# Kernel tuning notes

Measured on AMD Instinct MI355X. Metric: run time of the kernel, lower is better.

## Reference

```python
import jax, jax.numpy as jnp
import numpy as np

N = 100000
E = 1600000
BN_EPS = 1e-5
L2_EPS = 1e-12


def _sage_conv(x, src, dst, wl, bl, wr):
    # mean-aggregate source features onto destination nodes
    s = jax.ops.segment_sum(x[src], dst, num_segments=N)          # [N, C]
    cnt = jax.ops.segment_sum(jnp.ones((E,), x.dtype), dst, num_segments=N)
    agg = s / jnp.maximum(cnt, 1.0)[:, None]
    out = agg @ wl.T + bl + x @ wr.T                              # lin_l(agg) + lin_r(x)
    # normalize=True -> row-wise L2 normalization
    nrm = jnp.sqrt(jnp.sum(out * out, axis=-1, keepdims=True))
    return out / jnp.maximum(nrm, L2_EPS)


def _bn(x, g, b):
    # BatchNorm1d, training-mode batch statistics (biased variance)
    m = jnp.mean(x, axis=0)
    v = jnp.mean((x - m) ** 2, axis=0)
    return (x - m) / jnp.sqrt(v + BN_EPS) * g + b


def setup_inputs() -> dict:
    key = jax.random.key(0)
    ks = jax.random.split(key, 24)
    dims = [(4, 6), (6, 8), (8, 16), (16, 32)]
    inp = {
        "x": jax.random.normal(ks[0], (N, 4), jnp.float32),
        "edge_index": jax.random.randint(ks[1], (2, E), 0, N, dtype=jnp.int64),
    }
    ki = 2
    for li, (ci, co) in enumerate(dims, start=1):
        sc = 1.0 / np.sqrt(ci)
        inp[f"w{li}l"] = jax.random.uniform(ks[ki], (co, ci), jnp.float32, -sc, sc); ki += 1
        inp[f"b{li}l"] = jax.random.uniform(ks[ki], (co,), jnp.float32, -sc, sc); ki += 1
        inp[f"w{li}r"] = jax.random.uniform(ks[ki], (co, ci), jnp.float32, -sc, sc); ki += 1
    for li, co in enumerate([6, 8, 16], start=1):
        inp[f"g{li}"] = jnp.ones((co,), jnp.float32)
        inp[f"be{li}"] = jnp.zeros((co,), jnp.float32)
    return inp


def reference(x, edge_index,
              w1l, b1l, w1r, w2l, b2l, w2r, w3l, b3l, w3r, w4l, b4l, w4r,
              g1, be1, g2, be2, g3, be3):
    src, dst = edge_index[0], edge_index[1]
    h = _sage_conv(x, src, dst, w1l, b1l, w1r)
    h = _bn(jax.nn.relu(h), g1, be1)
    h = _sage_conv(h, src, dst, w2l, b2l, w2r)
    h = _bn(jax.nn.relu(h), g2, be2)
    h = _sage_conv(h, src, dst, w3l, b3l, w3r)
    h = _bn(jax.nn.relu(h), g3, be3)
    h = _sage_conv(h, src, dst, w4l, b4l, w4r)
    return jax.nn.relu(h)
```

## Files before the change

kernel.cpp:

```cpp
#include <hip/hip_runtime.h>

#define NNODES 100000
#define NEDGES 1600000
#define BN_EPS 1e-5f
#define L2_EPS 1e-12f

#define BKT_SHIFT 9
#define BKT_SIZE  512
#define NBKT      196
#define CHUNK     4096
#define NBLK_E    391

__global__ void hist_kernel(const int* __restrict__ dst,
                            int* __restrict__ blk_hist, float* __restrict__ stats) {
    __shared__ int h[NBKT];
    for (int i = threadIdx.x; i < NBKT; i += blockDim.x) h[i] = 0;
    if (blockIdx.x == 0 && threadIdx.x < 128) {
        stats[threadIdx.x] = 0.0f;
        stats[threadIdx.x + 128] = 0.0f;
        stats[threadIdx.x + 256] = 0.0f;
    }
    __syncthreads();
    int base = blockIdx.x * CHUNK;
    int end  = min(base + CHUNK, NEDGES);
    for (int e = base + threadIdx.x; e < end; e += blockDim.x)
        atomicAdd(&h[dst[e] >> BKT_SHIFT], 1);
    __syncthreads();
    for (int i = threadIdx.x; i < NBKT; i += blockDim.x)
        blk_hist[blockIdx.x * NBKT + i] = h[i];
}

__global__ void scan_blocks(const int* __restrict__ blk_hist,
                            int* __restrict__ blk_off, int* __restrict__ bucket_total) {
    __shared__ int tmp[512];
    int b = blockIdx.x;
    int i = threadIdx.x;
    int v = (i < NBLK_E) ? blk_hist[i * NBKT + b] : 0;
    tmp[i] = v;
    __syncthreads();
    for (int off = 1; off < 512; off <<= 1) {
        int t = (i >= off) ? tmp[i - off] : 0;
        __syncthreads();
        tmp[i] += t;
        __syncthreads();
    }
    if (i < NBLK_E) blk_off[i * NBKT + b] = tmp[i] - v;
    if (i == 511) bucket_total[b] = tmp[511];
}

__global__ void scan_buckets(const int* __restrict__ bucket_total, int* __restrict__ bucket_base) {
    __shared__ int tmp[256];
    int v = (threadIdx.x < NBKT) ? bucket_total[threadIdx.x] : 0;
    tmp[threadIdx.x] = v;
    __syncthreads();
    for (int off = 1; off < 256; off <<= 1) {
        int t = (threadIdx.x >= off) ? tmp[threadIdx.x - off] : 0;
        __syncthreads();
        tmp[threadIdx.x] += t;
        __syncthreads();
    }
    if (threadIdx.x < NBKT) bucket_base[threadIdx.x] = tmp[threadIdx.x] - v;
    if (threadIdx.x == 0) bucket_base[NBKT] = NEDGES;
}

__global__ void bucket_scatter(const int* __restrict__ src, const int* __restrict__ dst,
                               const int* __restrict__ blk_off, const int* __restrict__ bucket_base,
                               unsigned int* __restrict__ staged) {
    __shared__ int cur[NBKT];
    for (int i = threadIdx.x; i < NBKT; i += blockDim.x)
        cur[i] = blk_off[blockIdx.x * NBKT + i] + bucket_base[i];
    __syncthreads();
    int base = blockIdx.x * CHUNK;
    int end  = min(base + CHUNK, NEDGES);
    for (int e = base + threadIdx.x; e < end; e += blockDim.x) {
        int d = dst[e];
        int b = d >> BKT_SHIFT;
        int p = atomicAdd(&cur[b], 1);
        staged[p] = ((unsigned)(d & (BKT_SIZE - 1)) << 23) | (unsigned)src[e];
    }
}

__global__ void csr_finalize(const unsigned int* __restrict__ staged,
                             const int* __restrict__ bucket_base,
                             int* __restrict__ row_ptr, int* __restrict__ col) {
    __shared__ int nh[BKT_SIZE];
    __shared__ int cur[BKT_SIZE];
    int b = blockIdx.x;
    int beg = bucket_base[b], end = bucket_base[b + 1];

    nh[threadIdx.x] = 0;
    __syncthreads();
    for (int e = beg + threadIdx.x; e < end; e += blockDim.x)
        atomicAdd(&nh[staged[e] >> 23], 1);
    __syncthreads();

    int v = nh[threadIdx.x];
    cur[threadIdx.x] = v;
    __syncthreads();
    for (int off = 1; off < 512; off <<= 1) {
        int t = (threadIdx.x >= off) ? cur[threadIdx.x - off] : 0;
        __syncthreads();
        cur[threadIdx.x] += t;
        __syncthreads();
    }
    int excl = cur[threadIdx.x] - v;

    int node = b * BKT_SIZE + threadIdx.x;
    if (node < NNODES) row_ptr[node] = beg + excl;
    if (b == 0 && threadIdx.x == 0) row_ptr[NNODES] = NEDGES;
    __syncthreads();
    cur[threadIdx.x] = excl;
    __syncthreads();

    for (int e = beg + threadIdx.x; e < end; e += blockDim.x) {
        unsigned pk = staged[e];
        int l = (int)(pk >> 23);
        int p = atomicAdd(&cur[l], 1);
        col[beg + p] = (int)(pk & 0x7FFFFF);
    }
}

template<int CI>
__device__ __forceinline__ void load_row(const float* __restrict__ p, float* r) {
    constexpr int N4 = CI / 4;
#pragma unroll
    for (int i = 0; i < N4; i++) {
        float4 v = ((const float4*)p)[i];
        r[4*i] = v.x; r[4*i+1] = v.y; r[4*i+2] = v.z; r[4*i+3] = v.w;
    }
    if constexpr ((CI % 4) >= 2) {
        float2 v = ((const float2*)(p + 4 * N4))[0];
        r[4*N4] = v.x; r[4*N4+1] = v.y;
    }
    if constexpr ((CI % 2) == 1) r[CI - 1] = p[CI - 1];
}

template<int CI, int SI, int CO, int SO, int G, bool IN_AFFINE, bool DO_STATS>
__global__ void layer_kernel(const int* __restrict__ row_ptr, const int* __restrict__ col,
                             const float* __restrict__ h,
                             const float* __restrict__ ssum_in, const float* __restrict__ ssq_in,
                             const float* __restrict__ g_in, const float* __restrict__ b_in,
                             const float* __restrict__ wl, const float* __restrict__ bl,
                             const float* __restrict__ wr,
                             float* __restrict__ y,
                             float* __restrict__ stat_sum, float* __restrict__ stat_sq) {
    constexpr int NPB = 256 / G;
    constexpr int OPL = (CO + G - 1) / G;
    constexpr int PCI = CI + 1;

    __shared__ float sWl[CO * PCI];
    __shared__ float sWr[CO * PCI];
    __shared__ float sBl[CO];
    __shared__ float sSc[CI];
    __shared__ float sSh[CI];
    __shared__ float red_sum[CO];
    __shared__ float red_sq[CO];

    for (int i = threadIdx.x; i < CO * CI; i += blockDim.x) {
        int o = i / CI, c = i - o * CI;
        sWl[o * PCI + c] = wl[i];
        sWr[o * PCI + c] = wr[i];
    }
    if (threadIdx.x < CO) {
        sBl[threadIdx.x] = bl[threadIdx.x];
        if (DO_STATS) { red_sum[threadIdx.x] = 0.0f; red_sq[threadIdx.x] = 0.0f; }
    }
    if (IN_AFFINE && threadIdx.x < CI) {
        float m  = ssum_in[threadIdx.x] * (1.0f / NNODES);
        float vv = ssq_in[threadIdx.x] * (1.0f / NNODES) - m * m;
        float s  = g_in[threadIdx.x] / sqrtf(vv + BN_EPS);
        sSc[threadIdx.x] = s;
        sSh[threadIdx.x] = b_in[threadIdx.x] - m * s;
    }
    __syncthreads();

    int node = blockIdx.x * NPB + (threadIdx.x / G);
    int g    = threadIdx.x & (G - 1);
    bool valid = node < NNODES;

    float acc[CI];
#pragma unroll
    for (int c = 0; c < CI; c++) acc[c] = 0.0f;

    int beg = 0, end = 0;
    if (valid) {
        beg = row_ptr[node];
        end = row_ptr[node + 1];
        int j = beg + g;
        for (; j + 3 * G < end; j += 4 * G) {
            int i0 = col[j], i1 = col[j + G], i2 = col[j + 2 * G], i3 = col[j + 3 * G];
            float r0[CI], r1[CI], r2[CI], r3[CI];
            load_row<CI>(h + (long)i0 * SI, r0);
            load_row<CI>(h + (long)i1 * SI, r1);
            load_row<CI>(h + (long)i2 * SI, r2);
            load_row<CI>(h + (long)i3 * SI, r3);
#pragma unroll
            for (int c = 0; c < CI; c++) acc[c] += (r0[c] + r1[c]) + (r2[c] + r3[c]);
        }
        for (; j + G < end; j += 2 * G) {
            int i0 = col[j], i1 = col[j + G];
            float r0[CI], r1[CI];
            load_row<CI>(h + (long)i0 * SI, r0);
            load_row<CI>(h + (long)i1 * SI, r1);
#pragma unroll
            for (int c = 0; c < CI; c++) acc[c] += r0[c] + r1[c];
        }
        if (j < end) {
            float r0[CI];
            load_row<CI>(h + (long)col[j] * SI, r0);
#pragma unroll
            for (int c = 0; c < CI; c++) acc[c] += r0[c];
        }
    }

#pragma unroll
    for (int m = 1; m < G; m <<= 1)
#pragma unroll
        for (int c = 0; c < CI; c++) acc[c] += __shfl_xor(acc[c], m);

    float out[OPL];
    float nrm2 = 0.0f;
    if (valid) {
        float ic = 1.0f / fmaxf((float)(end - beg), 1.0f);
        float xin[CI];
        load_row<CI>(h + (long)node * SI, xin);
        float agg[CI];
#pragma unroll
        for (int c = 0; c < CI; c++) {
            float a  = acc[c] * ic;
            float xv = xin[c];
            if (IN_AFFINE) {
                a  = a  * sSc[c] + sSh[c];
                xv = xv * sSc[c] + sSh[c];
            }
            agg[c] = a;
            xin[c] = xv;
        }
#pragma unroll
        for (int k = 0; k < OPL; k++) {
            int o = g * OPL + k;
            float v = 0.0f;
            if (o < CO) {
                v = sBl[o];
#pragma unroll
                for (int c = 0; c < CI; c++)
                    v += sWl[o * PCI + c] * agg[c] + sWr[o * PCI + c] * xin[c];
            }
            out[k] = v;
            nrm2 += v * v;
        }
    }
#pragma unroll
    for (int m = 1; m < G; m <<= 1) nrm2 += __shfl_xor(nrm2, m);

    if (valid) {
        float inv_nrm = 1.0f / fmaxf(sqrtf(nrm2), L2_EPS);
#pragma unroll
        for (int k = 0; k < OPL; k++) {
            int o = g * OPL + k;
            if (o < CO) {
                float v = fmaxf(out[k] * inv_nrm, 0.0f);
                y[(long)node * SO + o] = v;
                if (DO_STATS) {
                    atomicAdd(&red_sum[o], v);
                    atomicAdd(&red_sq[o], v * v);
                }
            }
        }
    }

    if (DO_STATS) {
        __syncthreads();
        if (threadIdx.x < CO) {
            atomicAdd(&stat_sum[threadIdx.x], red_sum[threadIdx.x]);
            atomicAdd(&stat_sq[threadIdx.x], red_sq[threadIdx.x]);
        }
    }
}

extern "C" void kernel_launch(void* const* d_in, const int* in_sizes, int n_in,
                              void* d_out, int out_size, void* d_ws, size_t ws_size,
                              hipStream_t stream) {
    const float* x   = (const float*)d_in[0];
    const int*   ei  = (const int*)d_in[1];
    const int*   src = ei;
    const int*   dst = ei + NEDGES;

    const float* w1l = (const float*)d_in[2];
    const float* b1l = (const float*)d_in[3];
    const float* w1r = (const float*)d_in[4];
    const float* w2l = (const float*)d_in[5];
    const float* b2l = (const float*)d_in[6];
    const float* w2r = (const float*)d_in[7];
    const float* w3l = (const float*)d_in[8];
    const float* b3l = (const float*)d_in[9];
    const float* w3r = (const float*)d_in[10];
    const float* w4l = (const float*)d_in[11];
    const float* b4l = (const float*)d_in[12];
    const float* w4r = (const float*)d_in[13];
    const float* g1  = (const float*)d_in[14];
    const float* be1 = (const float*)d_in[15];
    const float* g2  = (const float*)d_in[16];
    const float* be2 = (const float*)d_in[17];
    const float* g3  = (const float*)d_in[18];
    const float* be3 = (const float*)d_in[19];

    char* w = (char*)d_ws;
    int* blk_hist     = (int*)w;  w += NBLK_E * NBKT * 4;
    int* blk_off      = (int*)w;  w += NBLK_E * NBKT * 4;
    int* bucket_total = (int*)w;  w += 256 * 4;
    int* bucket_base  = (int*)w;  w += 256 * 4;
    int* row_ptr      = (int*)w;  w += (NNODES + 8) * 4;
    int* col          = (int*)w;  w += NEDGES * 4;
    float* hA         = (float*)w; w += NNODES * 16 * 4;
    float* hB         = (float*)w; w += NNODES * 16 * 4;
    float* stats      = (float*)w; w += 3 * 128 * 4;
    unsigned int* staged = (unsigned int*)hB;

    float* ssum1 = stats + 0 * 128, *ssq1 = ssum1 + 32;
    float* ssum2 = stats + 1 * 128, *ssq2 = ssum2 + 32;
    float* ssum3 = stats + 2 * 128, *ssq3 = ssum3 + 32;

    hist_kernel   <<<NBLK_E, 256, 0, stream>>>(dst, blk_hist, stats);
    scan_blocks   <<<NBKT, 512, 0, stream>>>(blk_hist, blk_off, bucket_total);
    scan_buckets  <<<1, 256, 0, stream>>>(bucket_total, bucket_base);
    bucket_scatter<<<NBLK_E, 256, 0, stream>>>(src, dst, blk_off, bucket_base, staged);
    csr_finalize  <<<NBKT, 512, 0, stream>>>(staged, bucket_base, row_ptr, col);

    layer_kernel<4, 4, 6, 8, 4, false, true><<<(NNODES * 4 + 255) / 256, 256, 0, stream>>>(
        row_ptr, col, x, nullptr, nullptr, nullptr, nullptr,
        w1l, b1l, w1r, hA, ssum1, ssq1);

    layer_kernel<6, 8, 8, 8, 4, true, true><<<(NNODES * 4 + 255) / 256, 256, 0, stream>>>(
        row_ptr, col, hA, ssum1, ssq1, g1, be1,
        w2l, b2l, w2r, hB, ssum2, ssq2);

    layer_kernel<8, 8, 16, 16, 4, true, true><<<(NNODES * 4 + 255) / 256, 256, 0, stream>>>(
        row_ptr, col, hB, ssum2, ssq2, g2, be2,
        w3l, b3l, w3r, hA, ssum3, ssq3);

    layer_kernel<16, 16, 32, 32, 8, true, false><<<(NNODES * 8 + 255) / 256, 256, 0, stream>>>(
        row_ptr, col, hA, ssum3, ssq3, g3, be3,
        w4l, b4l, w4r, (float*)d_out, nullptr, nullptr);
}
```

Baseline: 276.4 us.

## Reorder nodes by in-degree within buckets to balance gather work

The CSR finalize kernel now counting-sorts the nodes of each 512-node bucket by in-degree and writes a permutation array. Each layer kernel maps its thread groups through this permutation, so groups in the same wavefront handle nodes with similar degrees and loop divergence drops. The cost is an extra indirection load per node, scattered output writes and row_ptr reads, and some extra shared-memory scan work in csr_finalize.

```diff
diff --git a/kernel.cpp b/kernel.cpp
--- a/kernel.cpp
+++ b/kernel.cpp
@@ -82,13 +82,17 @@
 
 __global__ void csr_finalize(const unsigned int* __restrict__ staged,
                              const int* __restrict__ bucket_base,
-                             int* __restrict__ row_ptr, int* __restrict__ col) {
+                             int* __restrict__ row_ptr, int* __restrict__ col,
+                             int* __restrict__ perm) {
     __shared__ int nh[BKT_SIZE];
     __shared__ int cur[BKT_SIZE];
+    __shared__ int dh[128];
+    __shared__ int dcur[128];
     int b = blockIdx.x;
     int beg = bucket_base[b], end = bucket_base[b + 1];
 
     nh[threadIdx.x] = 0;
+    if (threadIdx.x < 128) dh[threadIdx.x] = 0;
     __syncthreads();
     for (int e = beg + threadIdx.x; e < end; e += blockDim.x)
         atomicAdd(&nh[staged[e] >> 23], 1);
@@ -106,7 +110,8 @@
     int excl = cur[threadIdx.x] - v;
 
     int node = b * BKT_SIZE + threadIdx.x;
-    if (node < NNODES) row_ptr[node] = beg + excl;
+    bool node_valid = node < NNODES;
+    if (node_valid) row_ptr[node] = beg + excl;
     if (b == 0 && threadIdx.x == 0) row_ptr[NNODES] = NEDGES;
     __syncthreads();
     cur[threadIdx.x] = excl;
@@ -118,6 +123,24 @@
         int p = atomicAdd(&cur[l], 1);
         col[beg + p] = (int)(pk & 0x7FFFFF);
     }
+
+    int bin = min(v, 127);
+    if (node_valid) atomicAdd(&dh[bin], 1);
+    __syncthreads();
+    if (threadIdx.x < 128) dcur[threadIdx.x] = dh[threadIdx.x];
+    __syncthreads();
+    for (int off = 1; off < 128; off <<= 1) {
+        int t = (threadIdx.x < 128 && threadIdx.x >= off) ? dcur[threadIdx.x - off] : 0;
+        __syncthreads();
+        if (threadIdx.x < 128) dcur[threadIdx.x] += t;
+        __syncthreads();
+    }
+    if (threadIdx.x < 128) dcur[threadIdx.x] -= dh[threadIdx.x];
+    __syncthreads();
+    if (node_valid) {
+        int pos = atomicAdd(&dcur[bin], 1);
+        perm[b * BKT_SIZE + pos] = node;
+    }
 }
 
 template<int CI>
@@ -137,6 +160,7 @@
 
 template<int CI, int SI, int CO, int SO, int G, bool IN_AFFINE, bool DO_STATS>
 __global__ void layer_kernel(const int* __restrict__ row_ptr, const int* __restrict__ col,
+                             const int* __restrict__ perm,
                              const float* __restrict__ h,
                              const float* __restrict__ ssum_in, const float* __restrict__ ssq_in,
                              const float* __restrict__ g_in, const float* __restrict__ b_in,
@@ -174,9 +198,10 @@
     }
     __syncthreads();
 
-    int node = blockIdx.x * NPB + (threadIdx.x / G);
+    int gid  = blockIdx.x * NPB + (threadIdx.x / G);
     int g    = threadIdx.x & (G - 1);
-    bool valid = node < NNODES;
+    bool valid = gid < NNODES;
+    int node = valid ? perm[gid] : 0;
 
     float acc[CI];
 #pragma unroll
@@ -311,6 +336,7 @@
     int* bucket_total = (int*)w;  w += 256 * 4;
     int* bucket_base  = (int*)w;  w += 256 * 4;
     int* row_ptr      = (int*)w;  w += (NNODES + 8) * 4;
+    int* perm         = (int*)w;  w += NBKT * BKT_SIZE * 4;
     int* col          = (int*)w;  w += NEDGES * 4;
     float* hA         = (float*)w; w += NNODES * 16 * 4;
     float* hB         = (float*)w; w += NNODES * 16 * 4;
@@ -325,21 +351,21 @@
     scan_blocks   <<<NBKT, 512, 0, stream>>>(blk_hist, blk_off, bucket_total);
     scan_buckets  <<<1, 256, 0, stream>>>(bucket_total, bucket_base);
     bucket_scatter<<<NBLK_E, 256, 0, stream>>>(src, dst, blk_off, bucket_base, staged);
-    csr_finalize  <<<NBKT, 512, 0, stream>>>(staged, bucket_base, row_ptr, col);
+    csr_finalize  <<<NBKT, 512, 0, stream>>>(staged, bucket_base, row_ptr, col, perm);
 
     layer_kernel<4, 4, 6, 8, 4, false, true><<<(NNODES * 4 + 255) / 256, 256, 0, stream>>>(
-        row_ptr, col, x, nullptr, nullptr, nullptr, nullptr,
+        row_ptr, col, perm, x, nullptr, nullptr, nullptr, nullptr,
         w1l, b1l, w1r, hA, ssum1, ssq1);
 
     layer_kernel<6, 8, 8, 8, 4, true, true><<<(NNODES * 4 + 255) / 256, 256, 0, stream>>>(
-        row_ptr, col, hA, ssum1, ssq1, g1, be1,
+        row_ptr, col, perm, hA, ssum1, ssq1, g1, be1,
         w2l, b2l, w2r, hB, ssum2, ssq2);
 
     layer_kernel<8, 8, 16, 16, 4, true, true><<<(NNODES * 4 + 255) / 256, 256, 0, stream>>>(
-        row_ptr, col, hB, ssum2, ssq2, g2, be2,
+        row_ptr, col, perm, hB, ssum2, ssq2, g2, be2,
         w3l, b3l, w3r, hA, ssum3, ssq3);
 
     layer_kernel<16, 16, 32, 32, 8, true, false><<<(NNODES * 8 + 255) / 256, 256, 0, stream>>>(
-        row_ptr, col, hA, ssum3, ssq3, g3, be3,
+        row_ptr, col, perm, hA, ssum3, ssq3, g3, be3,
         w4l, b4l, w4r, (float*)d_out, nullptr, nullptr);
 }
```

After: 292.8 us. +5.9%, slower.

## Replace CSR build with bucketed edge lists and shared-memory atomic aggregation

Applied to the files above, without the earlier changes.

The per-node CSR finalize pass is dropped. Edges are bucketed into groups of 128 destination nodes, and each layer kernel walks the bucket's packed (local dst, src) list, accumulating neighbor features into a shared-memory tile with LDS float atomics. A small kernel precomputes inverse degrees. This removes the col/row_ptr construction and the sort within each bucket, but it adds heavy LDS atomic contention, only 782 blocks per layer, and an epilogue where only half the threads do the dense transform with one thread per node.

```diff
diff --git a/kernel.cpp b/kernel.cpp
--- a/kernel.cpp
+++ b/kernel.cpp
@@ -5,9 +5,9 @@
 #define BN_EPS 1e-5f
 #define L2_EPS 1e-12f
 
-#define BKT_SHIFT 9
-#define BKT_SIZE  512
-#define NBKT      196
+#define BKT_SHIFT 7
+#define BKT_SIZE  128
+#define NBKT      782
 #define CHUNK     4096
 #define NBLK_E    391
 
@@ -49,11 +49,11 @@
 }
 
 __global__ void scan_buckets(const int* __restrict__ bucket_total, int* __restrict__ bucket_base) {
-    __shared__ int tmp[256];
+    __shared__ int tmp[1024];
     int v = (threadIdx.x < NBKT) ? bucket_total[threadIdx.x] : 0;
     tmp[threadIdx.x] = v;
     __syncthreads();
-    for (int off = 1; off < 256; off <<= 1) {
+    for (int off = 1; off < 1024; off <<= 1) {
         int t = (threadIdx.x >= off) ? tmp[threadIdx.x - off] : 0;
         __syncthreads();
         tmp[threadIdx.x] += t;
@@ -76,67 +76,58 @@
         int d = dst[e];
         int b = d >> BKT_SHIFT;
         int p = atomicAdd(&cur[b], 1);
-        staged[p] = ((unsigned)(d & (BKT_SIZE - 1)) << 23) | (unsigned)src[e];
-    }
-}
-
-__global__ void csr_finalize(const unsigned int* __restrict__ staged,
-                             const int* __restrict__ bucket_base,
-                             int* __restrict__ row_ptr, int* __restrict__ col) {
-    __shared__ int nh[BKT_SIZE];
-    __shared__ int cur[BKT_SIZE];
+        staged[p] = ((unsigned)(d & (BKT_SIZE - 1)) << 25) | (unsigned)src[e];
+    }
+}
+
+__global__ void invdeg_kernel(const unsigned int* __restrict__ staged,
+                              const int* __restrict__ bucket_base,
+                              float* __restrict__ invdeg) {
+    __shared__ int deg[BKT_SIZE];
     int b = blockIdx.x;
+    if (threadIdx.x < BKT_SIZE) deg[threadIdx.x] = 0;
+    __syncthreads();
     int beg = bucket_base[b], end = bucket_base[b + 1];
-
-    nh[threadIdx.x] = 0;
-    __syncthreads();
     for (int e = beg + threadIdx.x; e < end; e += blockDim.x)
-        atomicAdd(&nh[staged[e] >> 23], 1);
-    __syncthreads();
-
-    int v = nh[threadIdx.x];
-    cur[threadIdx.x] = v;
-    __syncthreads();
-    for (int off = 1; off < 512; off <<= 1) {
-        int t = (threadIdx.x >= off) ? cur[threadIdx.x - off] : 0;
-        __syncthreads();
-        cur[threadIdx.x] += t;
-        __syncthreads();
-    }
-    int excl = cur[threadIdx.x] - v;
-
-    int node = b * BKT_SIZE + threadIdx.x;
-    if (node < NNODES) row_ptr[node] = beg + excl;
-    if (b == 0 && threadIdx.x == 0) row_ptr[NNODES] = NEDGES;
-    __syncthreads();
-    cur[threadIdx.x] = excl;
-    __syncthreads();
-
-    for (int e = beg + threadIdx.x; e < end; e += blockDim.x) {
-        unsigned pk = staged[e];
-        int l = (int)(pk >> 23);
-        int p = atomicAdd(&cur[l], 1);
-        col[beg + p] = (int)(pk & 0x7FFFFF);
-    }
-}
-
-template<int CI>
+        atomicAdd(&deg[staged[e] >> 25], 1);
+    __syncthreads();
+    if (threadIdx.x < BKT_SIZE) {
+        int node = b * BKT_SIZE + threadIdx.x;
+        if (node < NNODES)
+            invdeg[node] = 1.0f / fmaxf((float)deg[threadIdx.x], 1.0f);
+    }
+}
+
+template<int C>
 __device__ __forceinline__ void load_row(const float* __restrict__ p, float* r) {
-    constexpr int N4 = CI / 4;
+    constexpr int N4 = C / 4;
 #pragma unroll
     for (int i = 0; i < N4; i++) {
         float4 v = ((const float4*)p)[i];
         r[4*i] = v.x; r[4*i+1] = v.y; r[4*i+2] = v.z; r[4*i+3] = v.w;
     }
-    if constexpr ((CI % 4) >= 2) {
+    if constexpr ((C % 4) >= 2) {
         float2 v = ((const float2*)(p + 4 * N4))[0];
         r[4*N4] = v.x; r[4*N4+1] = v.y;
     }
-    if constexpr ((CI % 2) == 1) r[CI - 1] = p[CI - 1];
-}
-
-template<int CI, int SI, int CO, int SO, int G, bool IN_AFFINE, bool DO_STATS>
-__global__ void layer_kernel(const int* __restrict__ row_ptr, const int* __restrict__ col,
+    if constexpr ((C % 2) == 1) r[C - 1] = p[C - 1];
+}
+
+template<int C>
+__device__ __forceinline__ void store_row(float* __restrict__ p, const float* r) {
+    constexpr int N4 = C / 4;
+#pragma unroll
+    for (int i = 0; i < N4; i++)
+        ((float4*)p)[i] = make_float4(r[4*i], r[4*i+1], r[4*i+2], r[4*i+3]);
+    if constexpr ((C % 4) >= 2)
+        ((float2*)(p + 4 * N4))[0] = make_float2(r[4*N4], r[4*N4+1]);
+    if constexpr ((C % 2) == 1) p[C - 1] = r[C - 1];
+}
+
+template<int CI, int SI, int CO, int SO, bool IN_AFFINE, bool DO_STATS>
+__global__ void layer_kernel(const unsigned int* __restrict__ staged,
+                             const int* __restrict__ bucket_base,
+                             const float* __restrict__ invdeg,
                              const float* __restrict__ h,
                              const float* __restrict__ ssum_in, const float* __restrict__ ssq_in,
                              const float* __restrict__ g_in, const float* __restrict__ b_in,
@@ -144,10 +135,9 @@
                              const float* __restrict__ wr,
                              float* __restrict__ y,
                              float* __restrict__ stat_sum, float* __restrict__ stat_sq) {
-    constexpr int NPB = 256 / G;
-    constexpr int OPL = (CO + G - 1) / G;
     constexpr int PCI = CI + 1;
 
+    __shared__ float agg[BKT_SIZE * PCI];
     __shared__ float sWl[CO * PCI];
     __shared__ float sWr[CO * PCI];
     __shared__ float sBl[CO];
@@ -156,6 +146,7 @@
     __shared__ float red_sum[CO];
     __shared__ float red_sq[CO];
 
+    for (int i = threadIdx.x; i < BKT_SIZE * PCI; i += blockDim.x) agg[i] = 0.0f;
     for (int i = threadIdx.x; i < CO * CI; i += blockDim.x) {
         int o = i / CI, c = i - o * CI;
         sWl[o * PCI + c] = wl[i];
@@ -174,98 +165,77 @@
     }
     __syncthreads();
 
-    int node = blockIdx.x * NPB + (threadIdx.x / G);
-    int g    = threadIdx.x & (G - 1);
-    bool valid = node < NNODES;
-
-    float acc[CI];
-#pragma unroll
-    for (int c = 0; c < CI; c++) acc[c] = 0.0f;
-
-    int beg = 0, end = 0;
-    if (valid) {
-        beg = row_ptr[node];
-        end = row_ptr[node + 1];
-        int j = beg + g;
-        for (; j + 3 * G < end; j += 4 * G) {
-            int i0 = col[j], i1 = col[j + G], i2 = col[j + 2 * G], i3 = col[j + 3 * G];
-            float r0[CI], r1[CI], r2[CI], r3[CI];
-            load_row<CI>(h + (long)i0 * SI, r0);
-            load_row<CI>(h + (long)i1 * SI, r1);
-            load_row<CI>(h + (long)i2 * SI, r2);
-            load_row<CI>(h + (long)i3 * SI, r3);
-#pragma unroll
-            for (int c = 0; c < CI; c++) acc[c] += (r0[c] + r1[c]) + (r2[c] + r3[c]);
-        }
-        for (; j + G < end; j += 2 * G) {
-            int i0 = col[j], i1 = col[j + G];
-            float r0[CI], r1[CI];
-            load_row<CI>(h + (long)i0 * SI, r0);
-            load_row<CI>(h + (long)i1 * SI, r1);
-#pragma unroll
-            for (int c = 0; c < CI; c++) acc[c] += r0[c] + r1[c];
-        }
-        if (j < end) {
-            float r0[CI];
-            load_row<CI>(h + (long)col[j] * SI, r0);
-#pragma unroll
-            for (int c = 0; c < CI; c++) acc[c] += r0[c];
-        }
-    }
-
-#pragma unroll
-    for (int m = 1; m < G; m <<= 1)
-#pragma unroll
-        for (int c = 0; c < CI; c++) acc[c] += __shfl_xor(acc[c], m);
-
-    float out[OPL];
-    float nrm2 = 0.0f;
-    if (valid) {
-        float ic = 1.0f / fmaxf((float)(end - beg), 1.0f);
-        float xin[CI];
-        load_row<CI>(h + (long)node * SI, xin);
-        float agg[CI];
-#pragma unroll
-        for (int c = 0; c < CI; c++) {
-            float a  = acc[c] * ic;
-            float xv = xin[c];
-            if (IN_AFFINE) {
-                a  = a  * sSc[c] + sSh[c];
-                xv = xv * sSc[c] + sSh[c];
+    int b   = blockIdx.x;
+    int beg = bucket_base[b], end = bucket_base[b + 1];
+
+    int j = beg + threadIdx.x;
+    for (; j + 3 * 256 < end; j += 4 * 256) {
+        unsigned pk0 = staged[j], pk1 = staged[j + 256],
+                 pk2 = staged[j + 512], pk3 = staged[j + 768];
+        float r0[CI], r1[CI], r2[CI], r3[CI];
+        load_row<CI>(h + (long)(pk0 & 0x1FFFFFFu) * SI, r0);
+        load_row<CI>(h + (long)(pk1 & 0x1FFFFFFu) * SI, r1);
+        load_row<CI>(h + (long)(pk2 & 0x1FFFFFFu) * SI, r2);
+        load_row<CI>(h + (long)(pk3 & 0x1FFFFFFu) * SI, r3);
+        int l0 = pk0 >> 25, l1 = pk1 >> 25, l2 = pk2 >> 25, l3 = pk3 >> 25;
+#pragma unroll
+        for (int c = 0; c < CI; c++) atomicAdd(&agg[l0 * PCI + c], r0[c]);
+#pragma unroll
+        for (int c = 0; c < CI; c++) atomicAdd(&agg[l1 * PCI + c], r1[c]);
+#pragma unroll
+        for (int c = 0; c < CI; c++) atomicAdd(&agg[l2 * PCI + c], r2[c]);
+#pragma unroll
+        for (int c = 0; c < CI; c++) atomicAdd(&agg[l3 * PCI + c], r3[c]);
+    }
+    for (; j < end; j += 256) {
+        unsigned pk = staged[j];
+        float r0[CI];
+        load_row<CI>(h + (long)(pk & 0x1FFFFFFu) * SI, r0);
+        int l = pk >> 25;
+#pragma unroll
+        for (int c = 0; c < CI; c++) atomicAdd(&agg[l * PCI + c], r0[c]);
+    }
+    __syncthreads();
+
+    if (threadIdx.x < BKT_SIZE) {
+        int node = b * BKT_SIZE + threadIdx.x;
+        if (node < NNODES) {
+            float ic = invdeg[node];
+            float xin[CI], ag[CI];
+            load_row<CI>(h + (long)node * SI, xin);
+#pragma unroll
+            for (int c = 0; c < CI; c++) {
+                float a  = agg[threadIdx.x * PCI + c] * ic;
+                float xv = xin[c];
+                if (IN_AFFINE) {
+                    a  = a  * sSc[c] + sSh[c];
+                    xv = xv * sSc[c] + sSh[c];
+                }
+                ag[c]  = a;
+                xin[c] = xv;
             }
-            agg[c] = a;
-            xin[c] = xv;
-        }
-#pragma unroll
-        for (int k = 0; k < OPL; k++) {
-            int o = g * OPL + k;
-            float v = 0.0f;
-            if (o < CO) {
-                v = sBl[o];
+            float out[CO];
+            float nrm2 = 0.0f;
+#pragma unroll
+            for (int o = 0; o < CO; o++) {
+                float v = sBl[o];
 #pragma unroll
                 for (int c = 0; c < CI; c++)
-                    v += sWl[o * PCI + c] * agg[c] + sWr[o * PCI + c] * xin[c];
+                    v += sWl[o * PCI + c] * ag[c] + sWr[o * PCI + c] * xin[c];
+                out[o] = v;
+                nrm2 += v * v;
             }
-            out[k] = v;
-            nrm2 += v * v;
-        }
-    }
-#pragma unroll
-    for (int m = 1; m < G; m <<= 1) nrm2 += __shfl_xor(nrm2, m);
-
-    if (valid) {
-        float inv_nrm = 1.0f / fmaxf(sqrtf(nrm2), L2_EPS);
-#pragma unroll
-        for (int k = 0; k < OPL; k++) {
-            int o = g * OPL + k;
-            if (o < CO) {
-                float v = fmaxf(out[k] * inv_nrm, 0.0f);
-                y[(long)node * SO + o] = v;
+            float inv_nrm = 1.0f / fmaxf(sqrtf(nrm2), L2_EPS);
+#pragma unroll
+            for (int o = 0; o < CO; o++) {
+                float v = fmaxf(out[o] * inv_nrm, 0.0f);
+                out[o] = v;
                 if (DO_STATS) {
                     atomicAdd(&red_sum[o], v);
                     atomicAdd(&red_sq[o], v * v);
                 }
             }
+            store_row<CO>(y + (long)node * SO, out);
         }
     }
 
@@ -308,14 +278,13 @@
     char* w = (char*)d_ws;
     int* blk_hist     = (int*)w;  w += NBLK_E * NBKT * 4;
     int* blk_off      = (int*)w;  w += NBLK_E * NBKT * 4;
-    int* bucket_total = (int*)w;  w += 256 * 4;
-    int* bucket_base  = (int*)w;  w += 256 * 4;
-    int* row_ptr      = (int*)w;  w += (NNODES + 8) * 4;
-    int* col          = (int*)w;  w += NEDGES * 4;
+    int* bucket_total = (int*)w;  w += 1024 * 4;
+    int* bucket_base  = (int*)w;  w += 1024 * 4;
+    float* invdeg     = (float*)w; w += NNODES * 4;
+    unsigned int* staged = (unsigned int*)w; w += NEDGES * 4;
     float* hA         = (float*)w; w += NNODES * 16 * 4;
     float* hB         = (float*)w; w += NNODES * 16 * 4;
     float* stats      = (float*)w; w += 3 * 128 * 4;
-    unsigned int* staged = (unsigned int*)hB;
 
     float* ssum1 = stats + 0 * 128, *ssq1 = ssum1 + 32;
     float* ssum2 = stats + 1 * 128, *ssq2 = ssum2 + 32;
@@ -323,23 +292,23 @@
 
     hist_kernel   <<<NBLK_E, 256, 0, stream>>>(dst, blk_hist, stats);
     scan_blocks   <<<NBKT, 512, 0, stream>>>(blk_hist, blk_off, bucket_total);
-    scan_buckets  <<<1, 256, 0, stream>>>(bucket_total, bucket_base);
+    scan_buckets  <<<1, 1024, 0, stream>>>(bucket_total, bucket_base);
     bucket_scatter<<<NBLK_E, 256, 0, stream>>>(src, dst, blk_off, bucket_base, staged);
-    csr_finalize  <<<NBKT, 512, 0, stream>>>(staged, bucket_base, row_ptr, col);
-
-    layer_kernel<4, 4, 6, 8, 4, false, true><<<(NNODES * 4 + 255) / 256, 256, 0, stream>>>(
-        row_ptr, col, x, nullptr, nullptr, nullptr, nullptr,
+    invdeg_kernel <<<NBKT, 256, 0, stream>>>(staged, bucket_base, invdeg);
+
+    layer_kernel<4, 4, 6, 8, false, true><<<NBKT, 256, 0, stream>>>(
+        staged, bucket_base, invdeg, x, nullptr, nullptr, nullptr, nullptr,
         w1l, b1l, w1r, hA, ssum1, ssq1);
 
-    layer_kernel<6, 8, 8, 8, 4, true, true><<<(NNODES * 4 + 255) / 256, 256, 0, stream>>>(
-        row_ptr, col, hA, ssum1, ssq1, g1, be1,
+    layer_kernel<6, 8, 8, 8, true, true><<<NBKT, 256, 0, stream>>>(
+        staged, bucket_base, invdeg, hA, ssum1, ssq1, g1, be1,
         w2l, b2l, w2r, hB, ssum2, ssq2);
 
-    layer_kernel<8, 8, 16, 16, 4, true, true><<<(NNODES * 4 + 255) / 256, 256, 0, stream>>>(
-        row_ptr, col, hB, ssum2, ssq2, g2, be2,
+    layer_kernel<8, 8, 16, 16, true, true><<<NBKT, 256, 0, stream>>>(
+        staged, bucket_base, invdeg, hB, ssum2, ssq2, g2, be2,
         w3l, b3l, w3r, hA, ssum3, ssq3);
 
-    layer_kernel<16, 16, 32, 32, 8, true, false><<<(NNODES * 8 + 255) / 256, 256, 0, stream>>>(
-        row_ptr, col, hA, ssum3, ssq3, g3, be3,
+    layer_kernel<16, 16, 32, 32, true, false><<<NBKT, 256, 0, stream>>>(
+        staged, bucket_base, invdeg, hA, ssum3, ssq3, g3, be3,
         w4l, b4l, w4r, (float*)d_out, nullptr, nullptr);
 }
```

New measurement: 654.5 us. +136.8%, slower.

## Fuse four SAGE layer launches into one cooperative persistent kernel

Applied to the files above, without the earlier changes.

Replaces the four per-layer kernel launches with a single cooperative kernel that runs each layer in a grid-stride loop and separates layers with grid-wide syncs. This aims to remove the launch gaps and tail drain between layers. Per-block BN stat reductions now accumulate over many node tiles before the global atomic flush. It risks lower occupancy from combined shared memory and adds grid-sync cost, and it keeps the old multi-launch path as a fallback.

```diff
diff --git a/kernel.cpp b/kernel.cpp
--- a/kernel.cpp
+++ b/kernel.cpp
@@ -1,4 +1,7 @@
 #include <hip/hip_runtime.h>
+#include <hip/hip_cooperative_groups.h>
+
+namespace cg = cooperative_groups;
 
 #define NNODES 100000
 #define NEDGES 1600000
@@ -133,6 +136,153 @@
         r[4*N4] = v.x; r[4*N4+1] = v.y;
     }
     if constexpr ((CI % 2) == 1) r[CI - 1] = p[CI - 1];
+}
+
+template<int CI, int SI, int CO, int SO, int G, bool IN_AFFINE, bool DO_STATS>
+__device__ void layer_body(const int* __restrict__ row_ptr, const int* __restrict__ col,
+                           const float* __restrict__ h,
+                           const float* __restrict__ ssum_in, const float* __restrict__ ssq_in,
+                           const float* __restrict__ g_in, const float* __restrict__ b_in,
+                           const float* __restrict__ wl, const float* __restrict__ bl,
+                           const float* __restrict__ wr,
+                           float* __restrict__ y,
+                           float* __restrict__ stat_sum, float* __restrict__ stat_sq) {
+    constexpr int NPB = 256 / G;
+    constexpr int OPL = (CO + G - 1) / G;
+    constexpr int PCI = CI + 1;
+
+    __shared__ float sWl[CO * PCI];
+    __shared__ float sWr[CO * PCI];
+    __shared__ float sBl[CO];
+    __shared__ float sSc[CI];
+    __shared__ float sSh[CI];
+    __shared__ float red_sum[CO];
+    __shared__ float red_sq[CO];
+
+    for (int i = threadIdx.x; i < CO * CI; i += 256) {
+        int o = i / CI, c = i - o * CI;
+        sWl[o * PCI + c] = wl[i];
+        sWr[o * PCI + c] = wr[i];
+    }
+    if (threadIdx.x < CO) {
+        sBl[threadIdx.x] = bl[threadIdx.x];
+        if (DO_STATS) { red_sum[threadIdx.x] = 0.0f; red_sq[threadIdx.x] = 0.0f; }
+    }
+    if (IN_AFFINE && threadIdx.x < CI) {
+        float m  = ssum_in[threadIdx.x] * (1.0f / NNODES);
+        float vv = ssq_in[threadIdx.x] * (1.0f / NNODES) - m * m;
+        float s  = g_in[threadIdx.x] / sqrtf(vv + BN_EPS);
+        sSc[threadIdx.x] = s;
+        sSh[threadIdx.x] = b_in[threadIdx.x] - m * s;
+    }
+    __syncthreads();
+
+    const int NITER = (NNODES + NPB - 1) / NPB;
+    int g = threadIdx.x & (G - 1);
+
+    for (int vb = blockIdx.x; vb < NITER; vb += gridDim.x) {
+        int node = vb * NPB + (threadIdx.x / G);
+        bool valid = node < NNODES;
+
+        float acc[CI];
+#pragma unroll
+        for (int c = 0; c < CI; c++) acc[c] = 0.0f;
+
+        int beg = 0, end = 0;
+        if (valid) {
+            beg = row_ptr[node];
+            end = row_ptr[node + 1];
+            int j = beg + g;
+            for (; j + 3 * G < end; j += 4 * G) {
+                int i0 = col[j], i1 = col[j + G], i2 = col[j + 2 * G], i3 = col[j + 3 * G];
+                float r0[CI], r1[CI], r2[CI], r3[CI];
+                load_row<CI>(h + (long)i0 * SI, r0);
+                load_row<CI>(h + (long)i1 * SI, r1);
+                load_row<CI>(h + (long)i2 * SI, r2);
+                load_row<CI>(h + (long)i3 * SI, r3);
+#pragma unroll
+                for (int c = 0; c < CI; c++) acc[c] += (r0[c] + r1[c]) + (r2[c] + r3[c]);
+            }
+            for (; j + G < end; j += 2 * G) {
+                int i0 = col[j], i1 = col[j + G];
+                float r0[CI], r1[CI];
+                load_row<CI>(h + (long)i0 * SI, r0);
+                load_row<CI>(h + (long)i1 * SI, r1);
+#pragma unroll
+                for (int c = 0; c < CI; c++) acc[c] += r0[c] + r1[c];
+            }
+            if (j < end) {
+                float r0[CI];
+                load_row<CI>(h + (long)col[j] * SI, r0);
+#pragma unroll
+                for (int c = 0; c < CI; c++) acc[c] += r0[c];
+            }
+        }
+
+#pragma unroll
+        for (int m = 1; m < G; m <<= 1)
+#pragma unroll
+            for (int c = 0; c < CI; c++) acc[c] += __shfl_xor(acc[c], m);
+
+        float out[OPL];
+        float nrm2 = 0.0f;
+        if (valid) {
+            float ic = 1.0f / fmaxf((float)(end - beg), 1.0f);
+            float xin[CI];
+            load_row<CI>(h + (long)node * SI, xin);
+            float agg[CI];
+#pragma unroll
+            for (int c = 0; c < CI; c++) {
+                float a  = acc[c] * ic;
+                float xv = xin[c];
+                if (IN_AFFINE) {
+                    a  = a  * sSc[c] + sSh[c];
+                    xv = xv * sSc[c] + sSh[c];
+                }
+                agg[c] = a;
+                xin[c] = xv;
+            }
+#pragma unroll
+            for (int k = 0; k < OPL; k++) {
+                int o = g * OPL + k;
+                float v = 0.0f;
+                if (o < CO) {
+                    v = sBl[o];
+#pragma unroll
+                    for (int c = 0; c < CI; c++)
+                        v += sWl[o * PCI + c] * agg[c] + sWr[o * PCI + c] * xin[c];
+                }
+                out[k] = v;
+                nrm2 += v * v;
+            }
+        }
+#pragma unroll
+        for (int m = 1; m < G; m <<= 1) nrm2 += __shfl_xor(nrm2, m);
+
+        if (valid) {
+            float inv_nrm = 1.0f / fmaxf(sqrtf(nrm2), L2_EPS);
+#pragma unroll
+            for (int k = 0; k < OPL; k++) {
+                int o = g * OPL + k;
+                if (o < CO) {
+                    float v = fmaxf(out[k] * inv_nrm, 0.0f);
+                    y[(long)node * SO + o] = v;
+                    if (DO_STATS) {
+                        atomicAdd(&red_sum[o], v);
+                        atomicAdd(&red_sq[o], v * v);
+                    }
+                }
+            }
+        }
+    }
+
+    if (DO_STATS) {
+        __syncthreads();
+        if (threadIdx.x < CO) {
+            atomicAdd(&stat_sum[threadIdx.x], red_sum[threadIdx.x]);
+            atomicAdd(&stat_sq[threadIdx.x], red_sq[threadIdx.x]);
+        }
+    }
 }
 
 template<int CI, int SI, int CO, int SO, int G, bool IN_AFFINE, bool DO_STATS>
@@ -144,138 +294,52 @@
                              const float* __restrict__ wr,
                              float* __restrict__ y,
                              float* __restrict__ stat_sum, float* __restrict__ stat_sq) {
-    constexpr int NPB = 256 / G;
-    constexpr int OPL = (CO + G - 1) / G;
-    constexpr int PCI = CI + 1;
-
-    __shared__ float sWl[CO * PCI];
-    __shared__ float sWr[CO * PCI];
-    __shared__ float sBl[CO];
-    __shared__ float sSc[CI];
-    __shared__ float sSh[CI];
-    __shared__ float red_sum[CO];
-    __shared__ float red_sq[CO];
-
-    for (int i = threadIdx.x; i < CO * CI; i += blockDim.x) {
-        int o = i / CI, c = i - o * CI;
-        sWl[o * PCI + c] = wl[i];
-        sWr[o * PCI + c] = wr[i];
-    }
-    if (threadIdx.x < CO) {
-        sBl[threadIdx.x] = bl[threadIdx.x];
-        if (DO_STATS) { red_sum[threadIdx.x] = 0.0f; red_sq[threadIdx.x] = 0.0f; }
-    }
-    if (IN_AFFINE && threadIdx.x < CI) {
-        float m  = ssum_in[threadIdx.x] * (1.0f / NNODES);
-        float vv = ssq_in[threadIdx.x] * (1.0f / NNODES) - m * m;
-        float s  = g_in[threadIdx.x] / sqrtf(vv + BN_EPS);
-        sSc[threadIdx.x] = s;
-        sSh[threadIdx.x] = b_in[threadIdx.x] - m * s;
-    }
-    __syncthreads();
-
-    int node = blockIdx.x * NPB + (threadIdx.x / G);
-    int g    = threadIdx.x & (G - 1);
-    bool valid = node < NNODES;
-
-    float acc[CI];
-#pragma unroll
-    for (int c = 0; c < CI; c++) acc[c] = 0.0f;
-
-    int beg = 0, end = 0;
-    if (valid) {
-        beg = row_ptr[node];
-        end = row_ptr[node + 1];
-        int j = beg + g;
-        for (; j + 3 * G < end; j += 4 * G) {
-            int i0 = col[j], i1 = col[j + G], i2 = col[j + 2 * G], i3 = col[j + 3 * G];
-            float r0[CI], r1[CI], r2[CI], r3[CI];
-            load_row<CI>(h + (long)i0 * SI, r0);
-            load_row<CI>(h + (long)i1 * SI, r1);
-            load_row<CI>(h + (long)i2 * SI, r2);
-            load_row<CI>(h + (long)i3 * SI, r3);
-#pragma unroll
-            for (int c = 0; c < CI; c++) acc[c] += (r0[c] + r1[c]) + (r2[c] + r3[c]);
-        }
-        for (; j + G < end; j += 2 * G) {
-            int i0 = col[j], i1 = col[j + G];
-            float r0[CI], r1[CI];
-            load_row<CI>(h + (long)i0 * SI, r0);
-            load_row<CI>(h + (long)i1 * SI, r1);
-#pragma unroll
-            for (int c = 0; c < CI; c++) acc[c] += r0[c] + r1[c];
-        }
-        if (j < end) {
-            float r0[CI];
-            load_row<CI>(h + (long)col[j] * SI, r0);
-#pragma unroll
-            for (int c = 0; c < CI; c++) acc[c] += r0[c];
-        }
-    }
-
-#pragma unroll
-    for (int m = 1; m < G; m <<= 1)
-#pragma unroll
-        for (int c = 0; c < CI; c++) acc[c] += __shfl_xor(acc[c], m);
-
-    float out[OPL];
-    float nrm2 = 0.0f;
-    if (valid) {
-        float ic = 1.0f / fmaxf((float)(end - beg), 1.0f);
-        float xin[CI];
-        load_row<CI>(h + (long)node * SI, xin);
-        float agg[CI];
-#pragma unroll
-        for (int c = 0; c < CI; c++) {
-            float a  = acc[c] * ic;
-            float xv = xin[c];
-            if (IN_AFFINE) {
-                a  = a  * sSc[c] + sSh[c];
-                xv = xv * sSc[c] + sSh[c];
-            }
-            agg[c] = a;
-            xin[c] = xv;
-        }
-#pragma unroll
-        for (int k = 0; k < OPL; k++) {
-            int o = g * OPL + k;
-            float v = 0.0f;
-            if (o < CO) {
-                v = sBl[o];
-#pragma unroll
-                for (int c = 0; c < CI; c++)
-                    v += sWl[o * PCI + c] * agg[c] + sWr[o * PCI + c] * xin[c];
-            }
-            out[k] = v;
-            nrm2 += v * v;
-        }
-    }
-#pragma unroll
-    for (int m = 1; m < G; m <<= 1) nrm2 += __shfl_xor(nrm2, m);
-
-    if (valid) {
-        float inv_nrm = 1.0f / fmaxf(sqrtf(nrm2), L2_EPS);
-#pragma unroll
-        for (int k = 0; k < OPL; k++) {
-            int o = g * OPL + k;
-            if (o < CO) {
-                float v = fmaxf(out[k] * inv_nrm, 0.0f);
-                y[(long)node * SO + o] = v;
-                if (DO_STATS) {
-                    atomicAdd(&red_sum[o], v);
-                    atomicAdd(&red_sq[o], v * v);
-                }
-            }
-        }
-    }
-
-    if (DO_STATS) {
-        __syncthreads();
-        if (threadIdx.x < CO) {
-            atomicAdd(&stat_sum[threadIdx.x], red_sum[threadIdx.x]);
-            atomicAdd(&stat_sq[threadIdx.x], red_sq[threadIdx.x]);
-        }
-    }
+    layer_body<CI, SI, CO, SO, G, IN_AFFINE, DO_STATS>(
+        row_ptr, col, h, ssum_in, ssq_in, g_in, b_in, wl, bl, wr, y, stat_sum, stat_sq);
+}
+
+struct KParams {
+    const int* row_ptr; const int* col;
+    const float* x;
+    float* hA; float* hB;
+    float* stats;
+    const float* w1l; const float* b1l; const float* w1r;
+    const float* w2l; const float* b2l; const float* w2r;
+    const float* w3l; const float* b3l; const float* w3r;
+    const float* w4l; const float* b4l; const float* w4r;
+    const float* g1; const float* be1;
+    const float* g2; const float* be2;
+    const float* g3; const float* be3;
+    float* out;
+};
+
+__global__ void fused_layers(KParams p) {
+    cg::grid_group grid = cg::this_grid();
+    float* ssum1 = p.stats + 0 * 128, *ssq1 = ssum1 + 32;
+    float* ssum2 = p.stats + 1 * 128, *ssq2 = ssum2 + 32;
+    float* ssum3 = p.stats + 2 * 128, *ssq3 = ssum3 + 32;
+
+    layer_body<4, 4, 6, 8, 4, false, true>(
+        p.row_ptr, p.col, p.x, nullptr, nullptr, nullptr, nullptr,
+        p.w1l, p.b1l, p.w1r, p.hA, ssum1, ssq1);
+    __threadfence();
+    grid.sync();
+
+    layer_body<6, 8, 8, 8, 4, true, true>(
+        p.row_ptr, p.col, p.hA, ssum1, ssq1, p.g1, p.be1,
+        p.w2l, p.b2l, p.w2r, p.hB, ssum2, ssq2);
+    __threadfence();
+    grid.sync();
+
+    layer_body<8, 8, 16, 16, 4, true, true>(
+        p.row_ptr, p.col, p.hB, ssum2, ssq2, p.g2, p.be2,
+        p.w3l, p.b3l, p.w3r, p.hA, ssum3, ssq3);
+    __threadfence();
+    grid.sync();
+
+    layer_body<16, 16, 32, 32, 8, true, false>(
+        p.row_ptr, p.col, p.hA, ssum3, ssq3, p.g3, p.be3,
+        p.w4l, p.b4l, p.w4r, p.out, nullptr, nullptr);
 }
 
 extern "C" void kernel_launch(void* const* d_in, const int* in_sizes, int n_in,
@@ -285,25 +349,6 @@
     const int*   ei  = (const int*)d_in[1];
     const int*   src = ei;
     const int*   dst = ei + NEDGES;
-
-    const float* w1l = (const float*)d_in[2];
-    const float* b1l = (const float*)d_in[3];
-    const float* w1r = (const float*)d_in[4];
-    const float* w2l = (const float*)d_in[5];
-    const float* b2l = (const float*)d_in[6];
-    const float* w2r = (const float*)d_in[7];
-    const float* w3l = (const float*)d_in[8];
-    const float* b3l = (const float*)d_in[9];
-    const float* w3r = (const float*)d_in[10];
-    const float* w4l = (const float*)d_in[11];
-    const float* b4l = (const float*)d_in[12];
-    const float* w4r = (const float*)d_in[13];
-    const float* g1  = (const float*)d_in[14];
-    const float* be1 = (const float*)d_in[15];
-    const float* g2  = (const float*)d_in[16];
-    const float* be2 = (const float*)d_in[17];
-    const float* g3  = (const float*)d_in[18];
-    const float* be3 = (const float*)d_in[19];
 
     char* w = (char*)d_ws;
     int* blk_hist     = (int*)w;  w += NBLK_E * NBKT * 4;
@@ -327,19 +372,44 @@
     bucket_scatter<<<NBLK_E, 256, 0, stream>>>(src, dst, blk_off, bucket_base, staged);
     csr_finalize  <<<NBKT, 512, 0, stream>>>(staged, bucket_base, row_ptr, col);
 
-    layer_kernel<4, 4, 6, 8, 4, false, true><<<(NNODES * 4 + 255) / 256, 256, 0, stream>>>(
-        row_ptr, col, x, nullptr, nullptr, nullptr, nullptr,
-        w1l, b1l, w1r, hA, ssum1, ssq1);
-
-    layer_kernel<6, 8, 8, 8, 4, true, true><<<(NNODES * 4 + 255) / 256, 256, 0, stream>>>(
-        row_ptr, col, hA, ssum1, ssq1, g1, be1,
-        w2l, b2l, w2r, hB, ssum2, ssq2);
-
-    layer_kernel<8, 8, 16, 16, 4, true, true><<<(NNODES * 4 + 255) / 256, 256, 0, stream>>>(
-        row_ptr, col, hB, ssum2, ssq2, g2, be2,
-        w3l, b3l, w3r, hA, ssum3, ssq3);
-
-    layer_kernel<16, 16, 32, 32, 8, true, false><<<(NNODES * 8 + 255) / 256, 256, 0, stream>>>(
-        row_ptr, col, hA, ssum3, ssq3, g3, be3,
-        w4l, b4l, w4r, (float*)d_out, nullptr, nullptr);
-}
+    KParams p;
+    p.row_ptr = row_ptr; p.col = col; p.x = x;
+    p.hA = hA; p.hB = hB; p.stats = stats;
+    p.w1l = (const float*)d_in[2];  p.b1l = (const float*)d_in[3];  p.w1r = (const float*)d_in[4];
+    p.w2l = (const float*)d_in[5];  p.b2l = (const float*)d_in[6];  p.w2r = (const float*)d_in[7];
+    p.w3l = (const float*)d_in[8];  p.b3l = (const float*)d_in[9];  p.w3r = (const float*)d_in[10];
+    p.w4l = (const float*)d_in[11]; p.b4l = (const float*)d_in[12]; p.w4r = (const float*)d_in[13];
+    p.g1  = (const float*)d_in[14]; p.be1 = (const float*)d_in[15];
+    p.g2  = (const float*)d_in[16]; p.be2 = (const float*)d_in[17];
+    p.g3  = (const float*)d_in[18]; p.be3 = (const float*)d_in[19];
+    p.out = (float*)d_out;
+
+    int occ = 0;
+    hipError_t qerr = hipOccupancyMaxActiveBlocksPerMultiprocessor(
+        &occ, reinterpret_cast<const void*>(fused_layers), 256, 0);
+    bool coop_ok = (qerr == hipSuccess && occ >= 1);
+
+    if (coop_ok) {
+        int grid = occ * 256;
+        if (grid > 2048) grid = 2048;
+        void* args[] = { (void*)&p };
+        hipError_t lerr = hipLaunchCooperativeKernel(
+            reinterpret_cast<void*>(fused_layers), dim3(grid), dim3(256), args, 0, stream);
+        coop_ok = (lerr == hipSuccess);
+    }
+
+    if (!coop_ok) {
+        layer_kernel<4, 4, 6, 8, 4, false, true><<<(NNODES * 4 + 255) / 256, 256, 0, stream>>>(
+            row_ptr, col, x, nullptr, nullptr, nullptr, nullptr,
+            p.w1l, p.b1l, p.w1r, hA, ssum1, ssq1);
+        layer_kernel<6, 8, 8, 8, 4, true, true><<<(NNODES * 4 + 255) / 256, 256, 0, stream>>>(
+            row_ptr, col, hA, ssum1, ssq1, p.g1, p.be1,
+            p.w2l, p.b2l, p.w2r, hB, ssum2, ssq2);
+        layer_kernel<8, 8, 16, 16, 4, true, true><<<(NNODES * 4 + 255) / 256, 256, 0, stream>>>(
+            row_ptr, col, hB, ssum2, ssq2, p.g2, p.be2,
+            p.w3l, p.b3l, p.w3r, hA, ssum3, ssq3);
+        layer_kernel<16, 16, 32, 32, 8, true, false><<<(NNODES * 8 + 255) / 256, 256, 0, stream>>>(
+            row_ptr, col, hA, ssum3, ssq3, p.g3, p.be3,
+            p.w4l, p.b4l, p.w4r, (float*)d_out, nullptr, nullptr);
+    }
+}
```

After: 634.8 us. 2.3x slower.
